# Performance work log

Measured on AMD Instinct MI355X. Metric: run time of the kernel, lower is better.

Reference implementation:

```python
import jax, jax.numpy as jnp
import numpy as np
from jax import lax

B, N = 8, 261888          # images per GPU, anchors per image (1024x1024 FPN)
PRE_NMS = 6000            # config.PRE_NMS_LIMIT
NUM_PROP = 2000           # num_proposal
NMS_THRESH = 0.7
BBOX_STD = np.array([0.1, 0.1, 0.2, 0.2], np.float32)


def setup_inputs() -> dict:
    key = jax.random.key(0)
    k1, k2, k3, k4 = jax.random.split(key, 4)
    class_probs = jax.random.uniform(k1, (B, N, 2), dtype=jnp.float32)
    bbox_offset = jax.random.normal(k2, (B, N, 4), dtype=jnp.float32)
    # anchors in normalized [y1, x1, y2, x2] with y1<y2, x1<x2
    yx1 = jax.random.uniform(k3, (B, N, 2), dtype=jnp.float32) * 0.8
    hw = 0.02 + jax.random.uniform(k4, (B, N, 2), dtype=jnp.float32) * 0.18
    anchors = jnp.concatenate([yx1, yx1 + hw], axis=-1)
    return {"class_probs": class_probs, "bbox_offset": bbox_offset, "anchors": anchors}


def apply_bbox_offset(anc, deltas):
    h = anc[..., 2] - anc[..., 0]
    w = anc[..., 3] - anc[..., 1]
    cy = anc[..., 0] + 0.5 * h + deltas[..., 0] * h
    cx = anc[..., 1] + 0.5 * w + deltas[..., 1] * w
    h = h * jnp.exp(deltas[..., 2])
    w = w * jnp.exp(deltas[..., 3])
    return jnp.stack([cy - 0.5 * h, cx - 0.5 * w, cy + 0.5 * h, cx + 0.5 * w], axis=-1)


def iou_one_to_many(box, boxes):
    y1 = jnp.maximum(box[0], boxes[:, 0])
    x1 = jnp.maximum(box[1], boxes[:, 1])
    y2 = jnp.minimum(box[2], boxes[:, 2])
    x2 = jnp.minimum(box[3], boxes[:, 3])
    inter = jnp.maximum(y2 - y1, 0.0) * jnp.maximum(x2 - x1, 0.0)
    a1 = (box[2] - box[0]) * (box[3] - box[1])
    a2 = (boxes[:, 2] - boxes[:, 0]) * (boxes[:, 3] - boxes[:, 1])
    return inter / (a1 + a2 - inter + 1e-9)


def nms_single(boxes, scores):
    """Greedy NMS on [PRE_NMS,4] boxes (scores in [0,1]), padded to NUM_PROP."""
    n = boxes.shape[0]

    def step(valid, _):
        s = jnp.where(valid, scores, -1.0)
        idx = jnp.argmax(s)
        ok = s[idx] >= 0.0
        box = boxes[idx]
        ious = iou_one_to_many(box, boxes)
        new_valid = valid & (ious <= NMS_THRESH)
        new_valid = new_valid.at[idx].set(False)
        new_valid = jnp.where(ok, new_valid, valid)
        out_box = jnp.where(ok, box, jnp.zeros(4, boxes.dtype))
        return new_valid, out_box

    _, sel = lax.scan(step, jnp.ones(n, bool), None, length=NUM_PROP)
    return sel  # [NUM_PROP, 4], zero-padded


def reference(class_probs, bbox_offset, anchors):
    scores = class_probs[:, :, 1]                       # [B, N]
    deltas = bbox_offset * jnp.asarray(BBOX_STD)        # [B, N, 4]
    top_scores, ids = lax.top_k(scores, PRE_NMS)        # sorted descending
    gather4 = lambda a: jnp.take_along_axis(a, ids[..., None], axis=1)
    d = gather4(deltas)
    anc = gather4(anchors)
    boxes = jnp.clip(apply_bbox_offset(anc, d), 0.0, 1.0)  # clip to window [0,0,1,1]
    proposals = jax.vmap(nms_single)(boxes, top_scores)    # [B, NUM_PROP, 4]
    return proposals
```

## Files before the change

### kernel.cpp

```cpp
#include <hip/hip_runtime.h>
#include <stdint.h>


#define BATCH   8
#define NN      261888
#define PRE_NMS 6000
#define NUM_PROP 2000
#define CAND_CAP 8192
#define EDGE_CAP 16384
#define NTILE   94
#define NPAD    6016
#define NW32    188
#define NPAIRS  (NTILE*(NTILE+1)/2)
#define EWAVES  8

#define OFF_HIST1  4096
#define OFF_KEY    (OFF_HIST1 + BATCH*4096*4)
#define OFF_SBOX   OFF_HIST1
#define OFF_SORTED (OFF_SBOX + BATCH*NPAD*16)
#define OFF_BOXES  (OFF_SORTED + BATCH*PRE_NMS*4)
#define OFF_EDGES  (OFF_BOXES + BATCH*NPAD*16)
#define WS_NEED    (OFF_EDGES + BATCH*EDGE_CAP*4)
#define OFF_SORIG  OFF_SORTED
#define OFF_TMETA  (OFF_SORTED + 98304)
#define OFF_BSTART OFF_EDGES
#define OFF_BCUR   (OFF_EDGES + BATCH*4096*4)

#define CNT_EDGE(b)  (320 + (b)*32)

#define ZERO_U32   (OFF_KEY/4)

__device__ __forceinline__ uint32_t fkey(float s){
  uint32_t b = __float_as_uint(s);
  return (b & 0x80000000u) ? ~b : (b | 0x80000000u);
}

__device__ __forceinline__ int vbin(float s){
  int bin = (int)(s * 4096.0f);
  return bin < 0 ? 0 : (bin > 4095 ? 4095 : bin);
}

__device__ __forceinline__ uint64_t readlane64(uint64_t v, int src){
  uint32_t lo = __builtin_amdgcn_readlane((uint32_t)(v & 0xFFFFFFFFull), src);
  uint32_t hi = __builtin_amdgcn_readlane((uint32_t)(v >> 32), src);
  return (uint64_t)lo | ((uint64_t)hi << 32);
}

__device__ __forceinline__ uint32_t wave_reserve(bool pred, uint32_t* ctr){
  uint64_t m = __ballot((int)pred);
  if (!m) return 0xFFFFFFFFu;
  int lane = (int)(threadIdx.x & 63u);
  int leader = __ffsll((unsigned long long)m) - 1;
  uint32_t base = 0;
  if (lane == leader) base = atomicAdd(ctr, (uint32_t)__popcll(m));
  base = __shfl(base, leader, 64);
  return base + (uint32_t)__popcll(m & ((1ull << lane) - 1ull));
}

__global__ void k_zero(char* ws){
  int i = blockIdx.x*256 + threadIdx.x;
  if (i < ZERO_U32) ((uint32_t*)ws)[i] = 0u;
}

__global__ void k_histv(const float* __restrict__ probs, char* ws){
  __shared__ uint32_t h[4096];
  int b = blockIdx.y;
  for (int t = threadIdx.x; t < 4096; t += 256) h[t] = 0;
  __syncthreads();
  const float4* p4 = (const float4*)probs + (size_t)b * (NN/2);
  int base = blockIdx.x * 1024;
  for (int k = 0; k < 4; ++k){
    int m = base + k*256 + threadIdx.x;
    if (m < NN/2){
      float4 v = p4[m];
      atomicAdd(&h[vbin(v.y)], 1u);
      atomicAdd(&h[vbin(v.w)], 1u);
    }
  }
  __syncthreads();
  uint32_t* gh = (uint32_t*)(ws + OFF_HIST1) + b*4096;
  for (int t = threadIdx.x; t < 4096; t += 256) if (h[t]) atomicAdd(&gh[t], h[t]);
}

__global__ __launch_bounds__(256) void k_resolvev(char* ws){
  uint32_t* state = (uint32_t*)ws;
  __shared__ uint32_t h[4096];
  __shared__ uint32_t pfx[256];
  int b = blockIdx.x, t = threadIdx.x;
  const uint32_t* gh = (const uint32_t*)(ws + OFF_HIST1) + b*4096;
  for (int i = t; i < 4096; i += 256) h[i] = gh[i];
  __syncthreads();
  uint32_t s = 0;
  for (int k = 0; k < 16; ++k) s += h[t*16 + k];
  pfx[t] = s;
  __syncthreads();
  for (int d = 1; d < 256; d <<= 1){
    uint32_t v = (t >= d) ? pfx[t - d] : 0;
    __syncthreads();
    pfx[t] += v;
    __syncthreads();
  }
  uint32_t above = pfx[255] - pfx[t];
  uint32_t* bstart = (uint32_t*)(ws + OFF_BSTART);
  uint32_t* bcur   = (uint32_t*)(ws + OFF_BCUR);
  uint32_t run = above;
  for (int k = 15; k >= 0; --k){
    int bin = t*16 + k;
    uint32_t cnt = h[bin];
    bstart[bin*8 + b] = run;
    bcur[bin*8 + b] = run;
    if (run < PRE_NMS && run + cnt >= PRE_NMS){
      state[b] = (uint32_t)bin;
      state[8 + b] = run + cnt;
    }
    run += cnt;
  }
}

__global__ void k_compactv(const float* __restrict__ probs, char* ws){
  uint32_t* state = (uint32_t*)ws;
  uint64_t* keys  = (uint64_t*)(ws + OFF_KEY);
  uint32_t* bcur  = (uint32_t*)(ws + OFF_BCUR);
  int b = blockIdx.y;
  int c = (int)state[b];
  const float4* p4 = (const float4*)probs + (size_t)b * (NN/2);
  int base = blockIdx.x * 1024;
  for (int k = 0; k < 4; ++k){
    int m = base + k*256 + threadIdx.x;
    if (m < NN/2){
      float4 v = p4[m];
      int bin0 = vbin(v.y);
      if (bin0 >= c){
        uint32_t pos = atomicAdd(&bcur[bin0*8 + b], 1u);
        if (pos < CAND_CAP)
          keys[(size_t)b*CAND_CAP + pos] = ((uint64_t)fkey(v.y) << 32) | (uint32_t)(~(uint32_t)(2*m));
      }
      int bin1 = vbin(v.w);
      if (bin1 >= c){
        uint32_t pos = atomicAdd(&bcur[bin1*8 + b], 1u);
        if (pos < CAND_CAP)
          keys[(size_t)b*CAND_CAP + pos] = ((uint64_t)fkey(v.w) << 32) | (uint32_t)(~(uint32_t)(2*m + 1));
      }
    }
  }
}

__global__ __launch_bounds__(256) void k_rankgather(const float* __restrict__ boff,
                                                    const float* __restrict__ anc,
                                                    char* ws){
#pragma clang fp contract(off)
  uint32_t* state = (uint32_t*)ws;
  int b = blockIdx.y, t = threadIdx.x;
  uint32_t total = state[8 + b]; if (total > CAND_CAP) total = CAND_CAP;
  uint32_t kidx = blockIdx.x*256 + t;
  if (kidx >= total) return;
  const uint64_t* kb = (const uint64_t*)(ws + OFF_KEY) + (size_t)b * CAND_CAP;
  const uint32_t* bstart = (const uint32_t*)(ws + OFF_BSTART);
  const uint32_t* gh = (const uint32_t*)(ws + OFF_HIST1) + b*4096;
  uint64_t my = kb[kidx];
  float s = __uint_as_float((uint32_t)(my >> 32) & 0x7FFFFFFFu);
  int bin = vbin(s);
  uint32_t s0 = bstart[bin*8 + b];
  uint32_t e1 = s0 + gh[bin]; if (e1 > total) e1 = total;
  uint32_t rank = s0;
  for (uint32_t j = s0; j < e1; ++j) rank += (kb[j] > my) ? 1u : 0u;
  if (rank >= PRE_NMS) return;
  uint32_t id = ~(uint32_t)(my & 0xFFFFFFFFull);
  float4* boxes = (float4*)(ws + OFF_BOXES);
  float4 d4 = ((const float4*)boff)[(size_t)b*NN + id];
  float4 a4 = ((const float4*)anc )[(size_t)b*NN + id];
  float d0 = d4.x*0.1f, d1 = d4.y*0.1f, d2 = d4.z*0.2f, d3 = d4.w*0.2f;
  float h = a4.z - a4.x;
  float w = a4.w - a4.y;
  float cy = a4.x + 0.5f*h + d0*h;
  float cx = a4.y + 0.5f*w + d1*w;
  float h2 = h * expf(d2);
  float w2 = w * expf(d3);
  float y1 = cy - 0.5f*h2, x1 = cx - 0.5f*w2;
  float y2 = cy + 0.5f*h2, x2 = cx + 0.5f*w2;
  y1 = fminf(fmaxf(y1, 0.f), 1.f);
  x1 = fminf(fmaxf(x1, 0.f), 1.f);
  y2 = fminf(fmaxf(y2, 0.f), 1.f);
  x2 = fminf(fmaxf(x2, 0.f), 1.f);
  boxes[(size_t)b*NPAD + rank] = make_float4(y1, x1, y2, x2);
}

__global__ __launch_bounds__(1024) void k_cellsort(char* ws){
  __shared__ uint32_t hist[256];
  __shared__ uint32_t cur[256];
  __shared__ uint16_t cell[PRE_NMS];
  int b = blockIdx.x, t = threadIdx.x;
  const float4* boxes = (const float4*)(ws + OFF_BOXES) + (size_t)b*NPAD;
  float4* sbox = (float4*)(ws + OFF_SBOX) + (size_t)b*NPAD;
  uint16_t* sorig = (uint16_t*)(ws + OFF_SORIG) + (size_t)b*NPAD;
  float* tmeta = (float*)(ws + OFF_TMETA) + (size_t)b*NTILE*6;
  if (t < 256) hist[t] = 0;
  __syncthreads();
  for (int k = t; k < PRE_NMS; k += 1024){
    float4 bx = boxes[k];
    float cy = 0.5f*(bx.x + bx.z), cx = 0.5f*(bx.y + bx.w);
    int iy = (int)(cy*32.f); iy = iy < 0 ? 0 : (iy > 31 ? 31 : iy);
    int ix = (int)(cx*8.f);  ix = ix < 0 ? 0 : (ix > 7 ? 7 : ix);
    int c = (iy << 3) | ix;
    cell[k] = (uint16_t)c;
    atomicAdd(&hist[c], 1u);
  }
  __syncthreads();
  if (t < 256) cur[t] = hist[t];
  __syncthreads();
  for (int d = 1; d < 256; d <<= 1){
    uint32_t v = 0;
    if (t < 256 && t >= d) v = cur[t - d];
    __syncthreads();
    if (t < 256) cur[t] += v;
    __syncthreads();
  }
  if (t < 256) cur[t] -= hist[t];
  __syncthreads();
  for (int k = t; k < PRE_NMS; k += 1024){
    uint32_t slot = atomicAdd(&cur[cell[k]], 1u);
    sbox[slot] = boxes[k];
    sorig[slot] = (uint16_t)k;
  }
  for (int k = PRE_NMS + t; k < NPAD; k += 1024){
    sbox[k] = make_float4(3.f, 3.f, 3.f, 3.f);
    sorig[k] = 0;
  }
  __syncthreads();
  int wid = t >> 6, lane = t & 63;
  for (int tt = wid; tt < NTILE; tt += 16){
    float4 bx = sbox[tt*64 + lane];
    float cy = 0.5f*(bx.x + bx.z), cx = 0.5f*(bx.y + bx.w);
    float h = bx.z - bx.x, w = bx.w - bx.y;
    float cymin = cy, cymax = cy, cxmin = cx, cxmax = cx, hmax = h, wmax = w;
    for (int d = 32; d >= 1; d >>= 1){
      cymin = fminf(cymin, __shfl_xor(cymin, d));
      cymax = fmaxf(cymax, __shfl_xor(cymax, d));
      cxmin = fminf(cxmin, __shfl_xor(cxmin, d));
      cxmax = fmaxf(cxmax, __shfl_xor(cxmax, d));
      hmax  = fmaxf(hmax,  __shfl_xor(hmax,  d));
      wmax  = fmaxf(wmax,  __shfl_xor(wmax,  d));
    }
    if (lane == 0){
      tmeta[tt*6+0] = cymin; tmeta[tt*6+1] = cymax;
      tmeta[tt*6+2] = cxmin; tmeta[tt*6+3] = cxmax;
      tmeta[tt*6+4] = hmax;  tmeta[tt*6+5] = wmax;
    }
  }
}

__global__ __launch_bounds__(512) void k_edges(char* ws){
#pragma clang fp contract(off)
  const double M = 0x1.666667p-1;
  uint32_t* state = (uint32_t*)ws;
  const float4* sbox = (const float4*)(ws + OFF_SBOX);
  const uint16_t* sorig = (const uint16_t*)(ws + OFF_SORIG);
  const float* tmeta = (const float*)(ws + OFF_TMETA);
  uint32_t* edges = (uint32_t*)(ws + OFF_EDGES);
  __shared__ float4 cb[EWAVES][64];
  __shared__ float  ca[EWAVES][64];
  __shared__ uint16_t co[EWAVES][64];
  int b = blockIdx.y;
  int wid = (int)(threadIdx.x >> 6), t = (int)(threadIdx.x & 63u);
  int p0 = blockIdx.x*EWAVES + wid;
  if (p0 >= NPAIRS) return;
  float disc = (float)((2*NTILE+1)*(2*NTILE+1) - 8*p0);
  int ti = (int)(((float)(2*NTILE+1) - sqrtf(disc)) * 0.5f);
  if (ti < 0) ti = 0; if (ti > NTILE-1) ti = NTILE-1;
  while (ti+1 <= NTILE-1 && (ti+1)*NTILE - ((ti+1)*ti)/2 <= p0) ++ti;
  while (ti > 0 && ti*NTILE - (ti*(ti-1))/2 > p0) --ti;
  int tj = ti + (p0 - (ti*NTILE - (ti*(ti-1))/2));
  const float* mi = tmeta + ((size_t)b*NTILE + ti)*6;
  const float* mj = tmeta + ((size_t)b*NTILE + tj)*6;
  float gapy = fmaxf(fmaxf(mj[0] - mi[1], mi[0] - mj[1]), 0.f);
  float gapx = fmaxf(fmaxf(mj[2] - mi[3], mi[2] - mj[3]), 0.f);
  float by = 0.3015f*fminf(mi[4], mj[4]) + 2e-5f;
  float bx = 0.3015f*fminf(mi[5], mj[5]) + 2e-5f;
  if (gapy >= by || gapx >= bx) return;
  int j0 = tj*64 + t;
  float4 bj0 = sbox[(size_t)b*NPAD + j0];
  cb[wid][t] = bj0;
  ca[wid][t] = (bj0.z - bj0.x)*(bj0.w - bj0.y);
  co[wid][t] = sorig[(size_t)b*NPAD + j0];
  {
    float cyj = 0.5f*(bj0.x + bj0.z), cxj = 0.5f*(bj0.y + bj0.w);
    float hj = bj0.z - bj0.x, wj = bj0.w - bj0.y;
    float gy = fmaxf(fmaxf(mi[0] - cyj, cyj - mi[1]), 0.f);
    float gx = fmaxf(fmaxf(mi[2] - cxj, cxj - mi[3]), 0.f);
    bool plaus = (gy < 0.3015f*fminf(mi[4], hj) + 2e-5f) &&
                 (gx < 0.3015f*fminf(mi[5], wj) + 2e-5f);
    uint64_t jmask = __ballot((int)plaus);
    __builtin_amdgcn_s_waitcnt(0);
    int si = ti*64 + t;
    float4 bi = sbox[(size_t)b*NPAD + si];
    float ai = (bi.z - bi.x)*(bi.w - bi.y);
    uint32_t oi = sorig[(size_t)b*NPAD + si];
    uint64_t vm = (ti < tj) ? ~0ull : ((t == 63) ? 0ull : (~0ull << (t + 1)));
    uint64_t hitmask = 0;
    uint64_t jm = jmask;
    while (jm){
      int jj = __ffsll((unsigned long long)jm) - 1;
      jm &= jm - 1;
      float4 bj = cb[wid][jj];
      float yy1 = fmaxf(bi.x, bj.x);
      float xx1 = fmaxf(bi.y, bj.y);
      float yy2 = fminf(bi.z, bj.z);
      float xx2 = fminf(bi.w, bj.w);
      float ih = fmaxf(yy2 - yy1, 0.f);
      float iw = fmaxf(xx2 - xx1, 0.f);
      float inter = ih * iw;
      float uni = ai + ca[wid][jj] - inter + 1e-9f;
      bool hit = (double)inter >= M * (double)uni;
      hitmask |= hit ? (1ull << jj) : 0ull;
    }
    hitmask &= vm;
    while (__any((int)(hitmask != 0ull))){
      bool pred = hitmask != 0ull;
      int jj = pred ? (__ffsll((unsigned long long)hitmask) - 1) : 0;
      uint32_t slot = wave_reserve(pred, &state[CNT_EDGE(b)]);
      if (pred && slot < EDGE_CAP){
        uint32_t oj = co[wid][jj];
        uint32_t lo = oi < oj ? oi : oj;
        uint32_t hi = oi < oj ? oj : oi;
        edges[(size_t)b*EDGE_CAP + slot] = lo | (hi << 13);
      }
      hitmask &= hitmask - 1;
    }
  }
}

__global__ __launch_bounds__(256) void k_scan(char* ws, float* __restrict__ out){
  __shared__ uint32_t ebuf[EDGE_CAP];
  __shared__ uint32_t wdeg[NTILE + 1];
  __shared__ uint32_t woffs[NTILE + 1];
  __shared__ uint32_t wcur[NTILE];
  __shared__ uint32_t suppr[NW32];
  __shared__ uint32_t adjlo[64];
  __shared__ uint32_t adjhi[64];
  uint32_t* state = (uint32_t*)ws;
  const uint32_t* eb = (const uint32_t*)(ws + OFF_EDGES) + (size_t)blockIdx.x * EDGE_CAP;
  const float4* boxes = (const float4*)(ws + OFF_BOXES);
  int b = blockIdx.x, t = threadIdx.x;

  if (t <= NTILE) wdeg[t] = 0;
  for (int i = t; i < NW32; i += 256) suppr[i] = 0;
  __syncthreads();
  uint32_t E = state[CNT_EDGE(b)]; if (E > EDGE_CAP) E = EDGE_CAP;
  for (uint32_t e = t; e < E; e += 256)
    atomicAdd(&wdeg[(eb[e] & 0x1FFFu) >> 6], 1u);
  __syncthreads();
  if (t <= NTILE) woffs[t] = wdeg[t];
  __syncthreads();
  for (int d = 1; d <= NTILE; d <<= 1){
    uint32_t v = 0;
    if (t <= NTILE && t >= d) v = woffs[t - d];
    __syncthreads();
    if (t <= NTILE) woffs[t] += v;
    __syncthreads();
  }
  if (t <= NTILE){
    uint32_t ex = woffs[t] - wdeg[t];
    woffs[t] = ex;
    if (t < NTILE) wcur[t] = ex;
  }
  __syncthreads();
  for (uint32_t e = t; e < E; e += 256){
    uint32_t ed = eb[e];
    uint32_t ii = ed & 0x1FFFu, jj = ed >> 13;
    uint32_t slot = atomicAdd(&wcur[ii >> 6], 1u);
    ebuf[slot] = ((ii & 63u) << 16) | jj;
  }
  __syncthreads();
  if (t >= 64) return;
  int lane = t;
  uint32_t nsel = 0;
  float4 nbox = boxes[(size_t)b*NPAD + lane];
  for (int w = 0; w < NTILE && nsel < NUM_PROP; ++w){
    int base = w*64;
    float4 mybox = nbox;
    if (w + 1 < NTILE) nbox = boxes[(size_t)b*NPAD + base + 64 + lane];
    adjlo[lane] = 0; adjhi[lane] = 0;
    uint64_t sup = (uint64_t)suppr[2*w] | ((uint64_t)suppr[2*w + 1] << 32);
    uint64_t live = ~sup;
    int valid = PRE_NMS - base;
    if (valid < 64) live &= ((1ull << valid) - 1ull);
    uint32_t r0 = woffs[w], r1 = woffs[w + 1];
    bool anyIn = false;
    for (uint32_t idx = r0 + (uint32_t)lane; idx < r1; idx += 64){
      uint32_t e = ebuf[idx];
      uint32_t il = e >> 16, j = e & 0xFFFFu;
      if (((live >> il) & 1ull) && j < (uint32_t)(base + 64)){
        uint32_t l2 = j - (uint32_t)base;
        if (l2 < 32) atomicOr(&adjlo[il], 1u << l2);
        else         atomicOr(&adjhi[il], 1u << (l2 - 32));
        anyIn = true;
      }
    }
    anyIn = __any((int)anyIn);
    uint64_t sel;
    if (!anyIn){
      uint32_t cnt = __popcll(live);
      uint32_t remn = NUM_PROP - nsel;
      uint32_t take = cnt < remn ? cnt : remn;
      if (live & (1ull << lane)){
        uint32_t r = __popcll(live & ((1ull << lane) - 1ull));
        if (r < take) ((float4*)out)[(size_t)b*NUM_PROP + nsel + r] = mybox;
      }
      nsel += take;
      sel = live;
    } else {
      uint64_t row = (uint64_t)adjlo[lane] | ((uint64_t)adjhi[lane] << 32);
      uint64_t srcmask = __ballot((int)(row != 0ull));
      uint64_t m = live;
      sel = 0;
      while (m && nsel < NUM_PROP){
        uint64_t S = m & srcmask;
        int fS = S ? (__ffsll((unsigned long long)S) - 1) : 64;
        uint64_t below = (fS >= 64) ? ~0ull : ((1ull << fS) - 1ull);
        uint64_t freebits = m & below;
        if (freebits){
          uint32_t cnt = __popcll(freebits);
          uint32_t remn = NUM_PROP - nsel;
          uint32_t take = cnt < remn ? cnt : remn;
          if (freebits & (1ull << lane)){
            uint32_t r = __popcll(freebits & ((1ull << lane) - 1ull));
            if (r < take) ((float4*)out)[(size_t)b*NUM_PROP + nsel + r] = mybox;
          }
          nsel += take;
          sel |= freebits;
          m &= ~freebits;
          if (nsel >= NUM_PROP) break;
        }
        if (fS < 64){
          int fU = __builtin_amdgcn_readfirstlane(fS);
          if (lane == fU) ((float4*)out)[(size_t)b*NUM_PROP + nsel] = mybox;
          sel |= 1ull << fU;
          nsel++;
          m &= ~(1ull << fU);
          if (nsel >= NUM_PROP) break;
          m &= ~readlane64(row, fU);
        }
      }
    }
    if (nsel >= NUM_PROP) break;
    for (uint32_t idx = r0 + (uint32_t)lane; idx < r1; idx += 64){
      uint32_t e = ebuf[idx];
      uint32_t il = e >> 16, j = e & 0xFFFFu;
      if (((sel >> il) & 1ull) && j >= (uint32_t)(base + 64))
        atomicOr(&suppr[j >> 5], 1u << (j & 31));
    }
  }
  for (uint32_t r = nsel + (uint32_t)lane; r < NUM_PROP; r += 64)
    ((float4*)out)[(size_t)b*NUM_PROP + r] = make_float4(0.f, 0.f, 0.f, 0.f);
}

extern "C" void kernel_launch(void* const* d_in, const int* in_sizes, int n_in,
                              void* d_out, int out_size, void* d_ws, size_t ws_size,
                              hipStream_t stream){
  const float* probs = (const float*)d_in[0];
  const float* boff  = (const float*)d_in[1];
  const float* anc   = (const float*)d_in[2];
  char* ws = (char*)d_ws;
  float* out = (float*)d_out;

  k_zero      <<<(ZERO_U32 + 255)/256, 256, 0, stream>>>(ws);
  k_histv     <<<dim3(128, BATCH), 256, 0, stream>>>(probs, ws);
  k_resolvev  <<<BATCH, 256, 0, stream>>>(ws);
  k_compactv  <<<dim3(128, BATCH), 256, 0, stream>>>(probs, ws);
  k_rankgather<<<dim3(26, BATCH), 256, 0, stream>>>(boff, anc, ws);
  k_cellsort  <<<BATCH, 1024, 0, stream>>>(ws);
  k_edges     <<<dim3((NPAIRS + EWAVES - 1)/EWAVES, BATCH), 512, 0, stream>>>(ws);
  k_scan      <<<BATCH, 256, 0, stream>>>(ws, out);
}
```

Measured before the change: 142.2 us.

## Prefilter tile pairs into compact list before persistent edge kernel

Adds a k_prune kernel that tests every tile pair's bounding metadata and appends only plausibly overlapping pairs to a compact per-image list using a wave-level atomic reservation. k_edges becomes a grid-stride loop over that list with a fixed grid of 160 blocks per image, instead of launching one wave per tile pair and exiting early for most of them. This removes the large number of short-lived waves and their redundant pair-decode work, at the cost of an extra kernel launch and a global round trip for the pair list. The pair counter sits in the state area that the existing zero kernel is assumed to clear.

After: 142.9 us. Within noise of the previous version (+0.5%).

```diff
diff --git a/kernel.cpp b/kernel.cpp
--- a/kernel.cpp
+++ b/kernel.cpp
@@ -13,6 +13,7 @@
 #define NW32    188
 #define NPAIRS  (NTILE*(NTILE+1)/2)
 #define EWAVES  8
+#define PGRID   160
 
 #define OFF_HIST1  4096
 #define OFF_KEY    (OFF_HIST1 + BATCH*4096*4)
@@ -20,13 +21,15 @@
 #define OFF_SORTED (OFF_SBOX + BATCH*NPAD*16)
 #define OFF_BOXES  (OFF_SORTED + BATCH*PRE_NMS*4)
 #define OFF_EDGES  (OFF_BOXES + BATCH*NPAD*16)
-#define WS_NEED    (OFF_EDGES + BATCH*EDGE_CAP*4)
+#define OFF_PLIST  (OFF_EDGES + BATCH*EDGE_CAP*4)
+#define WS_NEED    (OFF_PLIST + BATCH*NPAIRS*4)
 #define OFF_SORIG  OFF_SORTED
 #define OFF_TMETA  (OFF_SORTED + 98304)
 #define OFF_BSTART OFF_EDGES
 #define OFF_BCUR   (OFF_EDGES + BATCH*4096*4)
 
 #define CNT_EDGE(b)  (320 + (b)*32)
+#define CNT_PAIR(b)  (576 + (b)*32)
 
 #define ZERO_U32   (OFF_KEY/4)
 
@@ -249,6 +252,30 @@
   }
 }
 
+__global__ __launch_bounds__(256) void k_prune(char* ws){
+  uint32_t* state = (uint32_t*)ws;
+  const float* tmeta = (const float*)(ws + OFF_TMETA);
+  uint32_t* plist = (uint32_t*)(ws + OFF_PLIST);
+  int b = blockIdx.y;
+  int p0 = blockIdx.x*256 + threadIdx.x;
+  bool ok = p0 < NPAIRS;
+  int ti = 0, tj = 0;
+  if (ok){
+    int p = p0;
+    while (p >= NTILE - ti){ p -= NTILE - ti; ++ti; }
+    tj = ti + p;
+    const float* mi = tmeta + ((size_t)b*NTILE + ti)*6;
+    const float* mj = tmeta + ((size_t)b*NTILE + tj)*6;
+    float gapy = fmaxf(fmaxf(mj[0] - mi[1], mi[0] - mj[1]), 0.f);
+    float gapx = fmaxf(fmaxf(mj[2] - mi[3], mi[2] - mj[3]), 0.f);
+    float by = 0.3015f*fminf(mi[4], mj[4]) + 2e-5f;
+    float bx = 0.3015f*fminf(mi[5], mj[5]) + 2e-5f;
+    ok = !(gapy >= by || gapx >= bx);
+  }
+  uint32_t slot = wave_reserve(ok, &state[CNT_PAIR(b)]);
+  if (ok) plist[(size_t)b*NPAIRS + slot] = ((uint32_t)ti << 8) | (uint32_t)tj;
+}
+
 __global__ __launch_bounds__(512) void k_edges(char* ws){
 #pragma clang fp contract(off)
   const double M = 0x1.666667p-1;
@@ -262,27 +289,17 @@
   __shared__ uint16_t co[EWAVES][64];
   int b = blockIdx.y;
   int wid = (int)(threadIdx.x >> 6), t = (int)(threadIdx.x & 63u);
-  int p0 = blockIdx.x*EWAVES + wid;
-  if (p0 >= NPAIRS) return;
-  float disc = (float)((2*NTILE+1)*(2*NTILE+1) - 8*p0);
-  int ti = (int)(((float)(2*NTILE+1) - sqrtf(disc)) * 0.5f);
-  if (ti < 0) ti = 0; if (ti > NTILE-1) ti = NTILE-1;
-  while (ti+1 <= NTILE-1 && (ti+1)*NTILE - ((ti+1)*ti)/2 <= p0) ++ti;
-  while (ti > 0 && ti*NTILE - (ti*(ti-1))/2 > p0) --ti;
-  int tj = ti + (p0 - (ti*NTILE - (ti*(ti-1))/2));
-  const float* mi = tmeta + ((size_t)b*NTILE + ti)*6;
-  const float* mj = tmeta + ((size_t)b*NTILE + tj)*6;
-  float gapy = fmaxf(fmaxf(mj[0] - mi[1], mi[0] - mj[1]), 0.f);
-  float gapx = fmaxf(fmaxf(mj[2] - mi[3], mi[2] - mj[3]), 0.f);
-  float by = 0.3015f*fminf(mi[4], mj[4]) + 2e-5f;
-  float bx = 0.3015f*fminf(mi[5], mj[5]) + 2e-5f;
-  if (gapy >= by || gapx >= bx) return;
-  int j0 = tj*64 + t;
-  float4 bj0 = sbox[(size_t)b*NPAD + j0];
-  cb[wid][t] = bj0;
-  ca[wid][t] = (bj0.z - bj0.x)*(bj0.w - bj0.y);
-  co[wid][t] = sorig[(size_t)b*NPAD + j0];
-  {
+  uint32_t cnt = state[CNT_PAIR(b)]; if (cnt > NPAIRS) cnt = NPAIRS;
+  const uint32_t* plist = (const uint32_t*)(ws + OFF_PLIST) + (size_t)b*NPAIRS;
+  for (uint32_t p0 = blockIdx.x*EWAVES + wid; p0 < cnt; p0 += PGRID*EWAVES){
+    uint32_t pe = plist[p0];
+    int ti = (int)(pe >> 8), tj = (int)(pe & 255u);
+    const float* mi = tmeta + ((size_t)b*NTILE + ti)*6;
+    int j0 = tj*64 + t;
+    float4 bj0 = sbox[(size_t)b*NPAD + j0];
+    cb[wid][t] = bj0;
+    ca[wid][t] = (bj0.z - bj0.x)*(bj0.w - bj0.y);
+    co[wid][t] = sorig[(size_t)b*NPAD + j0];
     float cyj = 0.5f*(bj0.x + bj0.z), cxj = 0.5f*(bj0.y + bj0.w);
     float hj = bj0.z - bj0.x, wj = bj0.w - bj0.y;
     float gy = fmaxf(fmaxf(mi[0] - cyj, cyj - mi[1]), 0.f);
@@ -469,6 +486,7 @@
   k_compactv  <<<dim3(128, BATCH), 256, 0, stream>>>(probs, ws);
   k_rankgather<<<dim3(26, BATCH), 256, 0, stream>>>(boff, anc, ws);
   k_cellsort  <<<BATCH, 1024, 0, stream>>>(ws);
-  k_edges     <<<dim3((NPAIRS + EWAVES - 1)/EWAVES, BATCH), 512, 0, stream>>>(ws);
+  k_prune     <<<dim3((NPAIRS + 255)/256, BATCH), 256, 0, stream>>>(ws);
+  k_edges     <<<dim3(PGRID, BATCH), 512, 0, stream>>>(ws);
   k_scan      <<<BATCH, 256, 0, stream>>>(ws, out);
 }
```
